# Kernel tuning notes

Hardware: AMD Instinct MI355X
Metric: run time of the kernel (lower is better)

## Reference

```python
import jax, jax.numpy as jnp
import numpy as np

H = 1000   # hidden_size
B = 64     # batch
S = 512    # encoder source length


def setup_inputs() -> dict:
    key = jax.random.key(0)
    ks = jax.random.split(key, 9)
    scale = 0.02
    return {
        "decoder_hidden": jax.random.normal(ks[0], (1, B, H), jnp.float32),
        "context": jax.random.normal(ks[1], (B, S, 2 * H), jnp.float32),
        "mask": jax.random.randint(ks[2], (B, S, 1), 0, 2) == 1,
        "W_a": jax.random.normal(ks[3], (H, 2 * H), jnp.float32) * scale,
        "W_b": jax.random.normal(ks[4], (H, H), jnp.float32) * scale,
        "W_c_w": jax.random.normal(ks[5], (1, H), jnp.float32) * scale,
        "W_c_b": jax.random.normal(ks[6], (1,), jnp.float32) * scale,
        "dense_w": jax.random.normal(ks[7], (H, 2 * H), jnp.float32) * scale,
        "dense_b": jax.random.normal(ks[8], (H,), jnp.float32) * scale,
    }


def reference(decoder_hidden, context, mask, W_a, W_b, W_c_w, W_c_b, dense_w, dense_b):
    # context_in: (B, S, H)
    context_in = jnp.einsum('bsd,hd->bsh', context, W_a)
    # hidden_in: (1, B, H) @ W_b.T -> transpose(0,1) -> (B, 1, H)
    hidden_in = jnp.transpose(jnp.einsum('nbd,hd->nbh', decoder_hidden, W_b), (1, 0, 2))
    # scores: (B, S, 1)
    attention = jnp.einsum('bsh,oh->bso', jnp.tanh(context_in + hidden_in), W_c_w) + W_c_b
    attention = jnp.where(mask, jnp.asarray(-1e6, attention.dtype), attention)
    attention_softmaxed = jax.nn.softmax(attention, axis=1)  # softmax over source length
    # weighted_sum: (B, 1, S) x (B, S, 2H) -> (B, 1, 2H)
    weighted_sum = jnp.einsum('bso,bsd->bod', attention_softmaxed, context)
    # dense: (B, 1, H)
    return jnp.einsum('bod,hd->boh', weighted_sum, dense_w) + dense_b
```

## Files before the change

kernel.cpp:

```cpp
#include <hip/hip_runtime.h>
#include <hip/hip_bf16.h>

#define H 1000
#define B 64
#define S 512
#define D 2000
#define KP 2048
#define NP 1024
#define MP 32768
#define KS 10

typedef __attribute__((ext_vector_type(8))) short short8;
typedef __attribute__((ext_vector_type(4))) float f32x4;

__device__ inline unsigned short f2bf(float f) {
  __hip_bfloat16 h = __float2bfloat16(f);
  union { __hip_bfloat16 h; unsigned short u; } c; c.h = h;
  return c.u;
}

__global__ __launch_bounds__(256) void k_hidden(const float* __restrict__ dec,
                                                const float* __restrict__ Wb,
                                                float* __restrict__ hi) {
  __shared__ float sdec[H];
  const int b = blockIdx.y;
  const int h = blockIdx.x * 4 + (threadIdx.x >> 6);
  const int lane = threadIdx.x & 63;
  for (int d = threadIdx.x; d < H; d += 256) sdec[d] = dec[b * H + d];
  __syncthreads();
  const float* w = Wb + (size_t)h * H;
  float acc = 0.f;
  for (int d = lane; d < H; d += 64) acc += w[d] * sdec[d];
  for (int o = 32; o; o >>= 1) acc += __shfl_xor(acc, o);
  if (lane == 0) hi[b * H + h] = acc;
}

__global__ __launch_bounds__(256) void k_cvt_t(const float* __restrict__ src,
                                               unsigned short* __restrict__ dst,
                                               int valid_rows) {
  __shared__ unsigned short st[4096];
  const int rp = blockIdx.x;
  const int tid = threadIdx.x;
  const int row = tid >> 2;
  const int kq = tid & 3;
  for (int t = blockIdx.y * 16; t < blockIdx.y * 16 + 16; ++t) {
    unsigned short v[2][8];
#pragma unroll
    for (int w = 0; w < 2; ++w) {
      const int r = row + w * 64;
      const int grow = rp * 128 + r;
      const int gcol = t * 32 + kq * 8;
      if (grow < valid_rows && gcol + 8 <= D) {
        const float* p = src + (size_t)grow * D + gcol;
        float4 x = *(const float4*)p;
        float4 y = *(const float4*)(p + 4);
        v[w][0] = f2bf(x.x); v[w][1] = f2bf(x.y); v[w][2] = f2bf(x.z); v[w][3] = f2bf(x.w);
        v[w][4] = f2bf(y.x); v[w][5] = f2bf(y.y); v[w][6] = f2bf(y.z); v[w][7] = f2bf(y.w);
      } else {
#pragma unroll
        for (int z = 0; z < 8; ++z) v[w][z] = 0;
      }
    }
    __syncthreads();
    *(short8*)&st[(kq * 128 + row) * 8] = *(short8*)&v[0][0];
    *(short8*)&st[(kq * 128 + row + 64) * 8] = *(short8*)&v[1][0];
    __syncthreads();
    unsigned short* ob = dst + ((size_t)rp * 64 + t) * 4096;
    *(short8*)(ob + tid * 8) = *(short8*)&st[tid * 8];
    *(short8*)(ob + 2048 + tid * 8) = *(short8*)&st[2048 + tid * 8];
  }
}

__global__ __launch_bounds__(256) void k_scores_fast(const unsigned short* __restrict__ ctxb,
                                                     const unsigned short* __restrict__ wab,
                                                     const float* __restrict__ hi,
                                                     const float* __restrict__ Wcw,
                                                     float* __restrict__ scores) {
  __shared__ unsigned short As[2][4096];
  __shared__ unsigned short Bs[2][4096];

  const int bid = blockIdx.x;
  const int swz = (bid & 7) * 256 + (bid >> 3);
  const int rtile = swz >> 3;
  const int ctile = swz & 7;
  const int row0 = rtile * 128;
  const int col0 = ctile * 128;

  const int tid = threadIdx.x;
  const int lane = tid & 63;
  const int wid = tid >> 6;
  const int wm = wid >> 1, wn = wid & 1;
  const int fr = lane & 15, fq = lane >> 4;

  const unsigned short* ga = ctxb + (size_t)rtile * (64 * 4096);
  const unsigned short* gb = wab + (size_t)ctile * (64 * 4096);

  f32x4 acc[4][4];
#pragma unroll
  for (int i = 0; i < 4; ++i)
#pragma unroll
    for (int j = 0; j < 4; ++j) acc[i][j] = (f32x4){0.f, 0.f, 0.f, 0.f};

#define STAGE(T, BUF)                                                                                      \
  do {                                                                                                     \
    const unsigned short* pa = ga + (size_t)(T) * 4096 + tid * 8;                                          \
    const unsigned short* pb = gb + (size_t)(T) * 4096 + tid * 8;                                          \
    __builtin_amdgcn_global_load_lds((const __attribute__((address_space(1))) unsigned int*)pa,            \
                                     (__attribute__((address_space(3))) unsigned int*)&As[BUF][tid * 8],   \
                                     16, 0, 0);                                                            \
    __builtin_amdgcn_global_load_lds((const __attribute__((address_space(1))) unsigned int*)(pa + 2048),   \
                                     (__attribute__((address_space(3))) unsigned int*)&As[BUF][tid * 8 + 2048], \
                                     16, 0, 0);                                                            \
    __builtin_amdgcn_global_load_lds((const __attribute__((address_space(1))) unsigned int*)pb,            \
                                     (__attribute__((address_space(3))) unsigned int*)&Bs[BUF][tid * 8],   \
                                     16, 0, 0);                                                            \
    __builtin_amdgcn_global_load_lds((const __attribute__((address_space(1))) unsigned int*)(pb + 2048),   \
                                     (__attribute__((address_space(3))) unsigned int*)&Bs[BUF][tid * 8 + 2048], \
                                     16, 0, 0);                                                            \
  } while (0)

  const int aoff = fq * 1024 + (wm * 64 + fr) * 8;
  const int boff = fq * 1024 + (wn * 64 + fr) * 8;

  STAGE(0, 0);
  __syncthreads();

  int buf = 0;
  for (int t = 0; t < 64; ++t) {
    if (t < 63) STAGE(t + 1, buf ^ 1);
    short8 a[4], bb[4];
#pragma unroll
    for (int mi = 0; mi < 4; ++mi) a[mi] = *(const short8*)&As[buf][aoff + mi * 128];
#pragma unroll
    for (int ni = 0; ni < 4; ++ni) bb[ni] = *(const short8*)&Bs[buf][boff + ni * 128];
#pragma unroll
    for (int mi = 0; mi < 4; ++mi)
#pragma unroll
      for (int ni = 0; ni < 4; ++ni)
        acc[mi][ni] = __builtin_amdgcn_mfma_f32_16x16x32_bf16(a[mi], bb[ni], acc[mi][ni], 0, 0, 0);
    __syncthreads();
    buf ^= 1;
  }
#undef STAGE

  const int b_idx = row0 >> 9;
  float wcv[4], hiv[4];
#pragma unroll
  for (int ni = 0; ni < 4; ++ni) {
    const int h = col0 + wn * 64 + ni * 16 + fr;
    wcv[ni] = (h < H) ? Wcw[h] : 0.f;
    hiv[ni] = (h < H) ? hi[b_idx * H + h] : 0.f;
  }
#pragma unroll
  for (int mi = 0; mi < 4; ++mi) {
#pragma unroll
    for (int r = 0; r < 4; ++r) {
      float p = 0.f;
#pragma unroll
      for (int ni = 0; ni < 4; ++ni)
        p += wcv[ni] * tanhf(acc[mi][ni][r] + hiv[ni]);
      p += __shfl_xor(p, 1);
      p += __shfl_xor(p, 2);
      p += __shfl_xor(p, 4);
      p += __shfl_xor(p, 8);
      if (fr == 0)
        atomicAdd(&scores[row0 + wm * 64 + mi * 16 + fq * 4 + r], p);
    }
  }
}

#define BM 128
#define BN 128
#define BK 32
#define NT 63
__global__ __launch_bounds__(256) void k_scores(const float* __restrict__ ctx,
                                                const float* __restrict__ Wa,
                                                const float* __restrict__ hi,
                                                const float* __restrict__ Wcw,
                                                float* __restrict__ scores) {
  __shared__ unsigned short As[2][BM][BK];
  __shared__ unsigned short Bs[2][BN][BK];

  const int bid = blockIdx.x;
  const int swz = (bid & 7) * 256 + (bid >> 3);
  const int row0 = (swz >> 3) * BM;
  const int col0 = (swz & 7) * BN;

  const int tid = threadIdx.x;
  const int lane = tid & 63;
  const int wid = tid >> 6;
  const int wm = wid >> 1;
  const int wn = wid & 1;
  const int fr = lane & 15;
  const int fq = lane >> 4;

  const int trow = tid >> 1;
  const int thalf = tid & 1;

  f32x4 acc[4][4];
#pragma unroll
  for (int i = 0; i < 4; ++i)
#pragma unroll
    for (int j = 0; j < 4; ++j) acc[i][j] = (f32x4){0.f, 0.f, 0.f, 0.f};

  const float* aptr = ctx + (size_t)(row0 + trow) * D + thalf * 16;
  const int hB = col0 + trow;
  const bool bvalid = (hB < H);
  const float* bptr = Wa + (size_t)(bvalid ? hB : 0) * D + thalf * 16;

  float4 ra[4], rb[4];

#define LOADT(T)                                                     \
  do {                                                               \
    const int base = (T) * BK + thalf * 16;                          \
    _Pragma("unroll")                                                \
    for (int q = 0; q < 4; ++q) {                                    \
      const int kk = base + q * 4;                                   \
      if (kk < D) {                                                  \
        ra[q] = *(const float4*)(aptr + (T) * BK + q * 4);           \
        if (bvalid) rb[q] = *(const float4*)(bptr + (T) * BK + q * 4); \
      }                                                              \
    }                                                                \
  } while (0)

#define CVTW(T, BUF)                                                 \
  do {                                                               \
    const int base = (T) * BK + thalf * 16;                          \
    unsigned short ta[16], tb[16];                                   \
    _Pragma("unroll")                                                \
    for (int q = 0; q < 4; ++q) {                                    \
      const int kk = base + q * 4;                                   \
      const bool v = (kk < D);                                       \
      ta[q * 4 + 0] = v ? f2bf(ra[q].x) : 0;                         \
      ta[q * 4 + 1] = v ? f2bf(ra[q].y) : 0;                         \
      ta[q * 4 + 2] = v ? f2bf(ra[q].z) : 0;                         \
      ta[q * 4 + 3] = v ? f2bf(ra[q].w) : 0;                         \
      const bool vb = v && bvalid;                                   \
      tb[q * 4 + 0] = vb ? f2bf(rb[q].x) : 0;                        \
      tb[q * 4 + 1] = vb ? f2bf(rb[q].y) : 0;                        \
      tb[q * 4 + 2] = vb ? f2bf(rb[q].z) : 0;                        \
      tb[q * 4 + 3] = vb ? f2bf(rb[q].w) : 0;                        \
    }                                                                \
    *(short8*)&As[BUF][trow][thalf * 16]     = *(short8*)&ta[0];     \
    *(short8*)&As[BUF][trow][thalf * 16 + 8] = *(short8*)&ta[8];     \
    *(short8*)&Bs[BUF][trow][thalf * 16]     = *(short8*)&tb[0];     \
    *(short8*)&Bs[BUF][trow][thalf * 16 + 8] = *(short8*)&tb[8];     \
  } while (0)

  LOADT(0);
  CVTW(0, 0);
  LOADT(1);
  __syncthreads();

  int cur = 0;
  for (int t = 0; t < NT; ++t) {
    short8 a[4], bbf[4];
#pragma unroll
    for (int mi = 0; mi < 4; ++mi)
      a[mi] = *(const short8*)&As[cur][wm * 64 + mi * 16 + fr][fq * 8];
#pragma unroll
    for (int ni = 0; ni < 4; ++ni)
      bbf[ni] = *(const short8*)&Bs[cur][wn * 64 + ni * 16 + fr][fq * 8];
#pragma unroll
    for (int mi = 0; mi < 4; ++mi)
#pragma unroll
      for (int ni = 0; ni < 4; ++ni)
        acc[mi][ni] = __builtin_amdgcn_mfma_f32_16x16x32_bf16(a[mi], bbf[ni], acc[mi][ni], 0, 0, 0);

    if (t + 1 < NT) {
      CVTW(t + 1, cur ^ 1);
      if (t + 2 < NT) LOADT(t + 2);
    }
    __syncthreads();
    cur ^= 1;
  }
#undef LOADT
#undef CVTW

  const int b_idx = row0 >> 9;
  float wcv[4], hiv[4];
#pragma unroll
  for (int ni = 0; ni < 4; ++ni) {
    const int h = col0 + wn * 64 + ni * 16 + fr;
    wcv[ni] = (h < H) ? Wcw[h] : 0.f;
    hiv[ni] = (h < H) ? hi[b_idx * H + h] : 0.f;
  }
#pragma unroll
  for (int mi = 0; mi < 4; ++mi) {
#pragma unroll
    for (int r = 0; r < 4; ++r) {
      float p = 0.f;
#pragma unroll
      for (int ni = 0; ni < 4; ++ni)
        p += wcv[ni] * tanhf(acc[mi][ni][r] + hiv[ni]);
      p += __shfl_xor(p, 1);
      p += __shfl_xor(p, 2);
      p += __shfl_xor(p, 4);
      p += __shfl_xor(p, 8);
      if (fr == 0)
        atomicAdd(&scores[row0 + wm * 64 + mi * 16 + fq * 4 + r], p);
    }
  }
}

__global__ __launch_bounds__(256) void k_softmax(const float* __restrict__ scores,
                                                 const int* __restrict__ mask,
                                                 const float* __restrict__ Wcb,
                                                 float* __restrict__ probs) {
  __shared__ float buf[S];
  __shared__ float rbuf[256];
  const int b = blockIdx.x;
  const float bias = Wcb[0];
  float mx = -3.4e38f;
  for (int s = threadIdx.x; s < S; s += 256) {
    float a = mask[b * S + s] ? -1e6f : (scores[b * S + s] + bias);
    buf[s] = a;
    mx = fmaxf(mx, a);
  }
  rbuf[threadIdx.x] = mx;
  __syncthreads();
  for (int w = 128; w > 0; w >>= 1) {
    if (threadIdx.x < w) rbuf[threadIdx.x] = fmaxf(rbuf[threadIdx.x], rbuf[threadIdx.x + w]);
    __syncthreads();
  }
  mx = rbuf[0];
  __syncthreads();
  float sum = 0.f;
  for (int s = threadIdx.x; s < S; s += 256) {
    float e = expf(buf[s] - mx);
    buf[s] = e;
    sum += e;
  }
  rbuf[threadIdx.x] = sum;
  __syncthreads();
  for (int w = 128; w > 0; w >>= 1) {
    if (threadIdx.x < w) rbuf[threadIdx.x] += rbuf[threadIdx.x + w];
    __syncthreads();
  }
  const float inv = 1.f / rbuf[0];
  for (int s = threadIdx.x; s < S; s += 256) probs[b * S + s] = buf[s] * inv;
}

__global__ __launch_bounds__(256) void k_wsum(const float* __restrict__ ctx,
                                              const float* __restrict__ probs,
                                              float* __restrict__ ws2) {
  __shared__ float p[S];
  const int b = blockIdx.y;
  const int d = blockIdx.x * 256 + threadIdx.x;
  for (int s = threadIdx.x; s < S; s += 256) p[s] = probs[b * S + s];
  __syncthreads();
  if (d < D) {
    float acc = 0.f;
    for (int s = 0; s < S; ++s) acc += p[s] * ctx[(size_t)(b * S + s) * D + d];
    ws2[b * D + d] = acc;
  }
}

__global__ __launch_bounds__(256) void k_dense_part(const float* __restrict__ ws2,
                                                    const float* __restrict__ Dw,
                                                    float* __restrict__ partial) {
  __shared__ float sw[64][201];
  const int tid = threadIdx.x;
  const int ks = blockIdx.y;
  const int k0 = ks * 200;
  for (int idx = tid; idx < 64 * 200; idx += 256) {
    const int b = idx / 200, k = idx - b * 200;
    sw[b][k] = ws2[(size_t)b * D + k0 + k];
  }
  __syncthreads();
  const int h = blockIdx.x * 4 + (tid >> 6);
  const int lane = tid & 63;
  const float* wrow = Dw + (size_t)h * D + k0;
  float acc = 0.f;
#pragma unroll 8
  for (int k = 0; k < 200; ++k) acc += wrow[k] * sw[lane][k];
  partial[((size_t)ks * 64 + lane) * 1000 + h] = acc;
}

__global__ __launch_bounds__(256) void k_dense_red(const float* __restrict__ partial,
                                                   const float* __restrict__ Db,
                                                   float* __restrict__ out) {
  const int idx = blockIdx.x * 256 + threadIdx.x;
  const int h = idx % 1000;
  float acc = Db[h];
#pragma unroll
  for (int ks = 0; ks < KS; ++ks) acc += partial[(size_t)ks * 64000 + idx];
  out[idx] = acc;
}

__global__ __launch_bounds__(256) void k_dense(const float* __restrict__ ws2,
                                               const float* __restrict__ Dw,
                                               const float* __restrict__ Db,
                                               float* __restrict__ out) {
  __shared__ float v[D];
  const int b = blockIdx.y;
  const int h = blockIdx.x * 256 + threadIdx.x;
  for (int d = threadIdx.x; d < D; d += 256) v[d] = ws2[b * D + d];
  __syncthreads();
  if (h < H) {
    const float* w = Dw + (size_t)h * D;
    float acc = 0.f;
    for (int d = 0; d < D; ++d) acc += w[d] * v[d];
    out[b * H + h] = acc + Db[h];
  }
}

extern "C" void kernel_launch(void* const* d_in, const int* in_sizes, int n_in,
                              void* d_out, int out_size, void* d_ws, size_t ws_size,
                              hipStream_t stream) {
  const float* dec = (const float*)d_in[0];
  const float* ctx = (const float*)d_in[1];
  const int*   mask = (const int*)d_in[2];
  const float* Wa  = (const float*)d_in[3];
  const float* Wb  = (const float*)d_in[4];
  const float* Wcw = (const float*)d_in[5];
  const float* Wcb = (const float*)d_in[6];
  const float* Dw  = (const float*)d_in[7];
  const float* Db  = (const float*)d_in[8];
  float* out = (float*)d_out;

  float* hi     = (float*)d_ws;
  float* scores = hi + B * H;
  float* probs  = scores + B * S;
  float* ws2    = probs + B * S;
  const size_t float_words = (size_t)B * H + 2 * B * S + B * D;
  unsigned short* ctx_b = (unsigned short*)((float*)d_ws + float_words);
  unsigned short* wa_b  = ctx_b + (size_t)MP * KP;
  float* partial = (float*)ctx_b;
  const size_t need = float_words * 4 + ((size_t)MP * KP + (size_t)NP * KP) * 2;

  hipMemsetAsync(scores, 0, B * S * sizeof(float), stream);
  k_hidden<<<dim3(250, B), 256, 0, stream>>>(dec, Wb, hi);
  if (ws_size >= need) {
    k_cvt_t<<<dim3(MP / 128, 4), 256, 0, stream>>>(ctx, ctx_b, MP);
    k_cvt_t<<<dim3(NP / 128, 4), 256, 0, stream>>>(Wa, wa_b, H);
    k_scores_fast<<<2048, 256, 0, stream>>>(ctx_b, wa_b, hi, Wcw, scores);
    k_softmax<<<B, 256, 0, stream>>>(scores, mask, Wcb, probs);
    k_wsum<<<dim3((D + 255) / 256, B), 256, 0, stream>>>(ctx, probs, ws2);
    k_dense_part<<<dim3(250, KS), 256, 0, stream>>>(ws2, Dw, partial);
    k_dense_red<<<250, 256, 0, stream>>>(partial, Db, out);
  } else {
    k_scores<<<2048, 256, 0, stream>>>(ctx, Wa, hi, Wcw, scores);
    k_softmax<<<B, 256, 0, stream>>>(scores, mask, Wcb, probs);
    k_wsum<<<dim3((D + 255) / 256, B), 256, 0, stream>>>(ctx, probs, ws2);
    k_dense<<<dim3((H + 255) / 256, B), 256, 0, stream>>>(ws2, Dw, Db, out);
  }
}
```

Baseline: 492.1 us.

## Triple-buffer scores GEMM, read bf16 context in wsum, batch hidden projection

The scores GEMM moves from double to triple LDS buffering, with explicit vmcnt waits, raw barriers and MFMA priority boosts, so global-to-LDS loads run further ahead of compute. The weighted sum now reads the already converted bf16 tiled context instead of the fp32 context, which halves the bytes read but adds bf16 rounding to that sum. The hidden projection is restructured around a transposed decoder state so each W_b row is read once for all batches rather than once per batch. These are three unrelated changes across different kernels, and dec_t reuses workspace memory that the conversion kernel later overwrites.

New measurement: 520.3 us. 1.06x slower.

```diff
diff --git a/kernel.cpp b/kernel.cpp
--- a/kernel.cpp
+++ b/kernel.cpp
@@ -17,6 +17,29 @@
   __hip_bfloat16 h = __float2bfloat16(f);
   union { __hip_bfloat16 h; unsigned short u; } c; c.h = h;
   return c.u;
+}
+__device__ inline float bf2f(unsigned short u) {
+  union { unsigned u; float f; } x; x.u = ((unsigned)u) << 16;
+  return x.f;
+}
+
+__global__ __launch_bounds__(256) void k_dect(const float* __restrict__ dec,
+                                              float* __restrict__ dec_t) {
+  const int d = blockIdx.x * 4 + (threadIdx.x >> 6);
+  const int b = threadIdx.x & 63;
+  dec_t[d * 64 + b] = dec[b * H + d];
+}
+
+__global__ __launch_bounds__(256) void k_hidden2(const float* __restrict__ dec_t,
+                                                 const float* __restrict__ Wb,
+                                                 float* __restrict__ hi) {
+  const int h = blockIdx.x * 4 + (threadIdx.x >> 6);
+  const int lane = threadIdx.x & 63;
+  const float* w = Wb + (size_t)h * H;
+  float acc = 0.f;
+#pragma unroll 4
+  for (int d = 0; d < H; ++d) acc += w[d] * dec_t[d * 64 + lane];
+  hi[lane * H + h] = acc;
 }
 
 __global__ __launch_bounds__(256) void k_hidden(const float* __restrict__ dec,
@@ -76,8 +99,8 @@
                                                      const float* __restrict__ hi,
                                                      const float* __restrict__ Wcw,
                                                      float* __restrict__ scores) {
-  __shared__ unsigned short As[2][4096];
-  __shared__ unsigned short Bs[2][4096];
+  __shared__ unsigned short As[3][4096];
+  __shared__ unsigned short Bs[3][4096];
 
   const int bid = blockIdx.x;
   const int swz = (bid & 7) * 256 + (bid >> 3);
@@ -122,26 +145,39 @@
   const int aoff = fq * 1024 + (wm * 64 + fr) * 8;
   const int boff = fq * 1024 + (wn * 64 + fr) * 8;
 
+#define COMPUTE(BI)                                                                     \
+  do {                                                                                  \
+    short8 a[4], bb[4];                                                                 \
+    _Pragma("unroll")                                                                   \
+    for (int mi = 0; mi < 4; ++mi) a[mi] = *(const short8*)&As[BI][aoff + mi * 128];    \
+    _Pragma("unroll")                                                                   \
+    for (int ni = 0; ni < 4; ++ni) bb[ni] = *(const short8*)&Bs[BI][boff + ni * 128];   \
+    __builtin_amdgcn_s_setprio(1);                                                      \
+    _Pragma("unroll")                                                                   \
+    for (int mi = 0; mi < 4; ++mi)                                                      \
+      _Pragma("unroll")                                                                 \
+      for (int ni = 0; ni < 4; ++ni)                                                    \
+        acc[mi][ni] = __builtin_amdgcn_mfma_f32_16x16x32_bf16(a[mi], bb[ni], acc[mi][ni], 0, 0, 0); \
+    __builtin_amdgcn_s_setprio(0);                                                      \
+  } while (0)
+
   STAGE(0, 0);
-  __syncthreads();
-
-  int buf = 0;
-  for (int t = 0; t < 64; ++t) {
-    if (t < 63) STAGE(t + 1, buf ^ 1);
-    short8 a[4], bb[4];
-#pragma unroll
-    for (int mi = 0; mi < 4; ++mi) a[mi] = *(const short8*)&As[buf][aoff + mi * 128];
-#pragma unroll
-    for (int ni = 0; ni < 4; ++ni) bb[ni] = *(const short8*)&Bs[buf][boff + ni * 128];
-#pragma unroll
-    for (int mi = 0; mi < 4; ++mi)
-#pragma unroll
-      for (int ni = 0; ni < 4; ++ni)
-        acc[mi][ni] = __builtin_amdgcn_mfma_f32_16x16x32_bf16(a[mi], bb[ni], acc[mi][ni], 0, 0, 0);
-    __syncthreads();
-    buf ^= 1;
-  }
+  STAGE(1, 1);
+  asm volatile("s_waitcnt vmcnt(4)" ::: "memory");
+  __builtin_amdgcn_s_barrier();
+
+  for (int t = 0; t < 62; ++t) {
+    STAGE(t + 2, (t + 2) % 3);
+    COMPUTE(t % 3);
+    asm volatile("s_waitcnt vmcnt(4)" ::: "memory");
+    __builtin_amdgcn_s_barrier();
+  }
+  COMPUTE(2);
+  asm volatile("s_waitcnt vmcnt(0)" ::: "memory");
+  __builtin_amdgcn_s_barrier();
+  COMPUTE(0);
 #undef STAGE
+#undef COMPUTE
 
   const int b_idx = row0 >> 9;
   float wcv[4], hiv[4];
@@ -341,6 +377,43 @@
   for (int s = threadIdx.x; s < S; s += 256) probs[b * S + s] = buf[s] * inv;
 }
 
+__global__ __launch_bounds__(256) void k_wsum_b(const unsigned short* __restrict__ ctxb,
+                                                const float* __restrict__ probs,
+                                                float* __restrict__ ws2) {
+  __shared__ float sp[S];
+  const int t = blockIdx.x;
+  const int b = blockIdx.y;
+  const int tid = threadIdx.x;
+  const int kq = tid >> 6;
+  const int lane = tid & 63;
+  for (int i = tid; i < S; i += 256) sp[i] = probs[b * S + i];
+  __syncthreads();
+  float acc[8];
+#pragma unroll
+  for (int e = 0; e < 8; ++e) acc[e] = 0.f;
+#pragma unroll
+  for (int rp4 = 0; rp4 < 4; ++rp4) {
+    const unsigned short* chunk = ctxb + ((size_t)(b * 4 + rp4) * 64 + t) * 4096;
+#pragma unroll
+    for (int w = 0; w < 2; ++w) {
+      const int row = lane + w * 64;
+      short8 v = *(const short8*)&chunk[(kq * 128 + row) * 8];
+      const float pv = sp[rp4 * 128 + row];
+#pragma unroll
+      for (int e = 0; e < 8; ++e) acc[e] += pv * bf2f((unsigned short)v[e]);
+    }
+  }
+#pragma unroll
+  for (int o = 32; o; o >>= 1)
+#pragma unroll
+    for (int e = 0; e < 8; ++e) acc[e] += __shfl_xor(acc[e], o);
+  const int d0 = t * 32 + kq * 8;
+  if (lane == 0 && d0 < D) {
+#pragma unroll
+    for (int e = 0; e < 8; ++e) ws2[(size_t)b * D + d0 + e] = acc[e];
+  }
+}
+
 __global__ __launch_bounds__(256) void k_wsum(const float* __restrict__ ctx,
                                               const float* __restrict__ probs,
                                               float* __restrict__ ws2) {
@@ -426,20 +499,23 @@
   const size_t float_words = (size_t)B * H + 2 * B * S + B * D;
   unsigned short* ctx_b = (unsigned short*)((float*)d_ws + float_words);
   unsigned short* wa_b  = ctx_b + (size_t)MP * KP;
+  float* dec_t  = (float*)ctx_b;
   float* partial = (float*)ctx_b;
   const size_t need = float_words * 4 + ((size_t)MP * KP + (size_t)NP * KP) * 2;
 
   hipMemsetAsync(scores, 0, B * S * sizeof(float), stream);
-  k_hidden<<<dim3(250, B), 256, 0, stream>>>(dec, Wb, hi);
   if (ws_size >= need) {
+    k_dect<<<250, 256, 0, stream>>>(dec, dec_t);
+    k_hidden2<<<250, 256, 0, stream>>>(dec_t, Wb, hi);
     k_cvt_t<<<dim3(MP / 128, 4), 256, 0, stream>>>(ctx, ctx_b, MP);
     k_cvt_t<<<dim3(NP / 128, 4), 256, 0, stream>>>(Wa, wa_b, H);
     k_scores_fast<<<2048, 256, 0, stream>>>(ctx_b, wa_b, hi, Wcw, scores);
     k_softmax<<<B, 256, 0, stream>>>(scores, mask, Wcb, probs);
-    k_wsum<<<dim3((D + 255) / 256, B), 256, 0, stream>>>(ctx, probs, ws2);
+    k_wsum_b<<<dim3(63, B), 256, 0, stream>>>(ctx_b, probs, ws2);
     k_dense_part<<<dim3(250, KS), 256, 0, stream>>>(ws2, Dw, partial);
     k_dense_red<<<250, 256, 0, stream>>>(partial, Db, out);
   } else {
+    k_hidden<<<dim3(250, B), 256, 0, stream>>>(dec, Wb, hi);
     k_scores<<<2048, 256, 0, stream>>>(ctx, Wa, hi, Wcw, scores);
     k_softmax<<<B, 256, 0, stream>>>(scores, mask, Wcb, probs);
     k_wsum<<<dim3((D + 255) / 256, B), 256, 0, stream>>>(ctx, probs, ws2);
```
